# Optimization experiments

Measured on AMD Instinct MI355X. Metric: run time of the kernel, lower is better.

Reference implementation:

```python
import jax, jax.numpy as jnp
import numpy as np
import math

Z, H, G, S = 4, 16, 4, 4096          # batch, q heads, kv groups, seq len
BLOCK = 32                            # compression block size
NB = S // BLOCK                       # number of compressed KV blocks (128)
DQK, DV = 128, 128                    # head dims


def setup_inputs() -> dict:
    key = jax.random.key(0)
    k1, k2, k3 = jax.random.split(key, 3)
    q = jax.random.normal(k1, (Z, H, S, DQK), jnp.float32)
    k_blocks = jax.random.normal(k2, (Z, G, NB, DQK), jnp.float32)
    v_blocks = jax.random.normal(k3, (Z, G, NB, DV), jnp.float32)
    # block j covers tokens [j*BLOCK, (j+1)*BLOCK), so it 'ends' at position (j+1)*BLOCK-1
    block_ends = (jnp.arange(1, NB + 1) * BLOCK - 1).astype(jnp.int32)
    return {"q": q, "k_blocks": k_blocks, "v_blocks": v_blocks, "block_ends": block_ends}


def reference(q, k_blocks, v_blocks, block_ends):
    """NSA compression attention fwd: block-end causal masking over compressed KV blocks.
    q: [Z,H,S,Dqk]; k_blocks/v_blocks: [Z,G,NB,D]; block_ends: [NB] int.
    Query at position m attends to compressed block j iff block_ends[j] <= m.
    Rows with no valid block output zeros (matching the kernel's l_i==0 path)."""
    Zb, Hb, Sb, Dq = q.shape
    Gb = k_blocks.shape[1]
    sm_scale = 1.0 / math.sqrt(Dq)
    # GQA: head h -> kv group h // (H // G)
    qg = (q * sm_scale).reshape(Zb, Gb, Hb // Gb, Sb, Dq)
    s = jnp.einsum('zghsd,zgnd->zghsn', qg, k_blocks)        # [Z,G,H/G,S,NB]
    pos = jnp.arange(Sb)
    mask = block_ends[None, :] <= pos[:, None]               # [S,NB]
    s_masked = jnp.where(mask, s, -jnp.inf)
    m = jnp.max(s_masked, axis=-1, keepdims=True)            # online-softmax max (M)
    m_safe = jnp.where(jnp.isfinite(m), m, 0.0)
    p = jnp.where(mask, jnp.exp(s_masked - jax.lax.stop_gradient(m_safe)), 0.0)
    l = jnp.sum(p, axis=-1, keepdims=True)                   # softmax denom (exp(L-M))
    o = jnp.einsum('zghsn,zgnv->zghsv', p, v_blocks)
    o = jnp.where(l > 0, o / jnp.where(l > 0, l, 1.0), 0.0)
    return o.reshape(Zb, Hb, Sb, -1)                         # [Z,H,S,Dv]
```

## Files before the change

kernel.cpp:

```cpp
#include <hip/hip_runtime.h>


#define Zc 4
#define Hc 16
#define Gc 4
#define Sc 4096
#define NBc 128
#define Dc 128
#define VST 136

typedef __attribute__((ext_vector_type(8))) short short8;
typedef __attribute__((ext_vector_type(4))) float float4v;

__device__ inline unsigned pk2bf(float a, float b) {
    union { float f; unsigned u; } x, y; x.f = a; y.f = b;
    return __builtin_amdgcn_perm(y.u + 0x8000u, x.u + 0x8000u, 0x07060302u);
}

__device__ inline short8 mkfrag(float4v f0, float4v f1) {
    union { short8 v; unsigned d[4]; } u;
    u.d[0] = pk2bf(f0[0], f0[1]);
    u.d[1] = pk2bf(f0[2], f0[3]);
    u.d[2] = pk2bf(f1[0], f1[1]);
    u.d[3] = pk2bf(f1[2], f1[3]);
    return u.v;
}

__global__ __launch_bounds__(256, 4)
void nsa_fwd(const float* __restrict__ q, const float* __restrict__ kb,
             const float* __restrict__ vb, float* __restrict__ out) {
    __shared__ __align__(16) short Vt[Dc * VST];

    const int m0   = blockIdx.x * 128;
    const int h    = blockIdx.y;
    const int z    = blockIdx.z;
    const int g    = h >> 2;
    const int tid  = threadIdx.x;
    const int wq   = tid >> 6;
    const int lane = tid & 63;
    const int l16  = lane & 15;
    const int quad = lane >> 4;

    const float* vsrc = vb + (size_t)(z * Gc + g) * NBc * Dc;
    #pragma unroll
    for (int it = 0; it < 16; it++) {
        int i = it * 256 + tid;
        int c = i >> 7, n = i & 127;
        float4v f = *(const float4v*)(vsrc + (size_t)n * Dc + c * 4);
        #pragma unroll
        for (int k2 = 0; k2 < 4; k2++) {
            union { float f; unsigned u; } x; x.f = f[k2];
            Vt[(c * 4 + k2) * VST + n] = (short)((x.u + 0x8000u) >> 16);
        }
    }

    const float* ksrc  = kb + (size_t)(z * Gc + g) * NBc * Dc;
    const float* qbase = q + ((size_t)(z * Hc + h) * Sc + m0 + wq * 32) * Dc;

    float4v acc[8][2];
    #pragma unroll
    for (int c = 0; c < 8; c++)
        #pragma unroll
        for (int t = 0; t < 2; t++) acc[c][t] = (float4v)0.f;

    #pragma unroll
    for (int dk = 0; dk < 4; dk++) {
        const int d0 = dk * 32 + quad * 8;
        short8 bq[2];
        #pragma unroll
        for (int t = 0; t < 2; t++) {
            const float* s = qbase + (size_t)(t * 16 + l16) * Dc + d0;
            bq[t] = mkfrag(*(const float4v*)s, *(const float4v*)(s + 4));
        }
        #pragma unroll
        for (int c = 0; c < 8; c++) {
            const float* s = ksrc + (size_t)(c * 16 + l16) * Dc + d0;
            short8 a = mkfrag(*(const float4v*)s, *(const float4v*)(s + 4));
            #pragma unroll
            for (int t = 0; t < 2; t++)
                acc[c][t] = __builtin_amdgcn_mfma_f32_16x16x32_bf16(
                    a, bq[t], acc[c][t], 0, 0, 0);
        }
    }

    const float sm_scale = 0.08838834764831845f;
    unsigned Ppk[8][2][2];
    #pragma unroll
    for (int t = 0; t < 2; t++) {
        const int mg = m0 + wq * 32 + t * 16 + l16;
        int nv = (mg + 1) >> 5; if (nv > NBc) nv = NBc;
        float mx = -1e30f;
        #pragma unroll
        for (int c = 0; c < 8; c++)
            #pragma unroll
            for (int r = 0; r < 4; r++) {
                const int j = c * 16 + quad * 4 + r;
                float s = acc[c][t][r] * sm_scale;
                s = (j < nv) ? s : -1e30f;
                acc[c][t][r] = s;
                mx = fmaxf(mx, s);
            }
        mx = fmaxf(mx, __shfl_xor(mx, 16, 64));
        mx = fmaxf(mx, __shfl_xor(mx, 32, 64));
        float ls = 0.f;
        #pragma unroll
        for (int c = 0; c < 8; c++)
            #pragma unroll
            for (int r = 0; r < 4; r++) {
                float s = acc[c][t][r];
                float p = (s > -1e29f) ? __expf(s - mx) : 0.f;
                acc[c][t][r] = p;
                ls += p;
            }
        ls += __shfl_xor(ls, 16, 64);
        ls += __shfl_xor(ls, 32, 64);
        const float inv = (ls > 0.f) ? 1.f / ls : 0.f;
        #pragma unroll
        for (int c = 0; c < 8; c++) {
            Ppk[c][t][0] = pk2bf(acc[c][t][0] * inv, acc[c][t][1] * inv);
            Ppk[c][t][1] = pk2bf(acc[c][t][2] * inv, acc[c][t][3] * inv);
        }
    }

    __syncthreads();

    float4v oacc[8][2];
    #pragma unroll
    for (int c = 0; c < 8; c++)
        #pragma unroll
        for (int t = 0; t < 2; t++) oacc[c][t] = (float4v)0.f;

    const int s0 = (((2 * quad) & 3) << 4) | l16;
    const int s1 = (((2 * quad + 1) & 3) << 4) | l16;
    const bool hi = (quad >= 2);

    #pragma unroll
    for (int kbi = 0; kbi < 4; kbi++) {
        short8 ap[2];
        #pragma unroll
        for (int t = 0; t < 2; t++) {
            const int c1 = 2 * kbi;
            unsigned w0a = (unsigned)__shfl((int)Ppk[c1    ][t][0], s0, 64);
            unsigned w0b = (unsigned)__shfl((int)Ppk[c1 + 1][t][0], s0, 64);
            unsigned w1a = (unsigned)__shfl((int)Ppk[c1    ][t][1], s0, 64);
            unsigned w1b = (unsigned)__shfl((int)Ppk[c1 + 1][t][1], s0, 64);
            unsigned w2a = (unsigned)__shfl((int)Ppk[c1    ][t][0], s1, 64);
            unsigned w2b = (unsigned)__shfl((int)Ppk[c1 + 1][t][0], s1, 64);
            unsigned w3a = (unsigned)__shfl((int)Ppk[c1    ][t][1], s1, 64);
            unsigned w3b = (unsigned)__shfl((int)Ppk[c1 + 1][t][1], s1, 64);
            union { short8 v; unsigned d[4]; } u;
            u.d[0] = hi ? w0b : w0a;
            u.d[1] = hi ? w1b : w1a;
            u.d[2] = hi ? w2b : w2a;
            u.d[3] = hi ? w3b : w3a;
            ap[t] = u.v;
        }
        #pragma unroll
        for (int c = 0; c < 8; c++) {
            short8 bv = *(const short8*)(Vt + (c * 16 + l16) * VST + kbi * 32 + quad * 8);
            #pragma unroll
            for (int t = 0; t < 2; t++)
                oacc[c][t] = __builtin_amdgcn_mfma_f32_16x16x32_bf16(
                    ap[t], bv, oacc[c][t], 0, 0, 0);
        }
    }

    float* obase = out + ((size_t)(z * Hc + h) * Sc + m0 + wq * 32) * Dc;
    #pragma unroll
    for (int t = 0; t < 2; t++)
        #pragma unroll
        for (int rr = 0; rr < 4; rr++) {
            const int row = t * 16 + quad * 4 + rr;
            #pragma unroll
            for (int c = 0; c < 8; c++)
                obase[(size_t)row * Dc + c * 16 + l16] = oacc[c][t][rr];
        }
}

extern "C" void kernel_launch(void* const* d_in, const int* in_sizes, int n_in,
                              void* d_out, int out_size, void* d_ws, size_t ws_size,
                              hipStream_t stream) {
    const float* q  = (const float*)d_in[0];
    const float* kb = (const float*)d_in[1];
    const float* vb = (const float*)d_in[2];
    float* out = (float*)d_out;
    dim3 grid(Sc / 128, Hc, Zc);
    nsa_fwd<<<grid, dim3(256), 0, stream>>>(q, kb, vb, out);
}
```

Before: 296.1 us.

## Stage bf16 K in shared memory, preload Q, and skip causally masked blocks

K blocks are converted to bf16 once per workgroup into shared memory instead of each wave reloading and converting them from global memory. Q fragments are loaded early and pre-scaled by the softmax scale. Per-tile bounds derived from the causal block mask skip QK and PV MFMAs and softmax work for key blocks that are fully masked. The cost is doubled LDS use and occupancy lowered from 4 to 2 blocks per CU in launch bounds, plus more registers held for the preloaded Q.

```diff
diff --git a/kernel.cpp b/kernel.cpp
--- a/kernel.cpp
+++ b/kernel.cpp
@@ -16,7 +16,6 @@
     union { float f; unsigned u; } x, y; x.f = a; y.f = b;
     return __builtin_amdgcn_perm(y.u + 0x8000u, x.u + 0x8000u, 0x07060302u);
 }
-
 __device__ inline short8 mkfrag(float4v f0, float4v f1) {
     union { short8 v; unsigned d[4]; } u;
     u.d[0] = pk2bf(f0[0], f0[1]);
@@ -26,21 +25,44 @@
     return u.v;
 }
 
-__global__ __launch_bounds__(256, 4)
+__global__ __launch_bounds__(256, 2)
 void nsa_fwd(const float* __restrict__ q, const float* __restrict__ kb,
              const float* __restrict__ vb, float* __restrict__ out) {
+    __shared__ __align__(16) short Ksh[NBc * VST];
     __shared__ __align__(16) short Vt[Dc * VST];
 
-    const int m0   = blockIdx.x * 128;
-    const int h    = blockIdx.y;
-    const int z    = blockIdx.z;
-    const int g    = h >> 2;
+    const int bx   = blockIdx.x, m0 = bx * 128;
+    const int h    = blockIdx.y, z = blockIdx.z, g = h >> 2;
     const int tid  = threadIdx.x;
     const int wq   = tid >> 6;
     const int lane = tid & 63;
     const int l16  = lane & 15;
     const int quad = lane >> 4;
 
+    const int nvmax   = 4 * bx + 4;
+    const int c_max   = (nvmax + 15) >> 4;
+    const int kbi_max = (nvmax + 31) >> 5;
+
+    const float* qbase = q + ((size_t)(z * Hc + h) * Sc + m0 + wq * 32) * Dc;
+    float4v qraw[4][2][2];
+    #pragma unroll
+    for (int dk = 0; dk < 4; dk++)
+        #pragma unroll
+        for (int t = 0; t < 2; t++) {
+            const float* s = qbase + (size_t)(t * 16 + l16) * Dc + dk * 32 + quad * 8;
+            qraw[dk][t][0] = *(const float4v*)s;
+            qraw[dk][t][1] = *(const float4v*)(s + 4);
+        }
+
+    const float* ksrc = kb + (size_t)(z * Gc + g) * NBc * Dc;
+    #pragma unroll
+    for (int it = 0; it < 8; it++) {
+        int i = it * 256 + tid;
+        int n = i >> 4, c8 = i & 15;
+        const float* s = ksrc + (size_t)n * Dc + c8 * 8;
+        float4v f0 = *(const float4v*)s, f1 = *(const float4v*)(s + 4);
+        *(short8*)(Ksh + n * VST + c8 * 8) = mkfrag(f0, f1);
+    }
     const float* vsrc = vb + (size_t)(z * Gc + g) * NBc * Dc;
     #pragma unroll
     for (int it = 0; it < 16; it++) {
@@ -54,8 +76,15 @@
         }
     }
 
-    const float* ksrc  = kb + (size_t)(z * Gc + g) * NBc * Dc;
-    const float* qbase = q + ((size_t)(z * Hc + h) * Sc + m0 + wq * 32) * Dc;
+    const float sm = 0.08838834764831845f;
+    short8 qf[4][2];
+    #pragma unroll
+    for (int dk = 0; dk < 4; dk++)
+        #pragma unroll
+        for (int t = 0; t < 2; t++)
+            qf[dk][t] = mkfrag(qraw[dk][t][0] * sm, qraw[dk][t][1] * sm);
+
+    __syncthreads();
 
     float4v acc[8][2];
     #pragma unroll
@@ -64,27 +93,21 @@
         for (int t = 0; t < 2; t++) acc[c][t] = (float4v)0.f;
 
     #pragma unroll
-    for (int dk = 0; dk < 4; dk++) {
-        const int d0 = dk * 32 + quad * 8;
-        short8 bq[2];
-        #pragma unroll
-        for (int t = 0; t < 2; t++) {
-            const float* s = qbase + (size_t)(t * 16 + l16) * Dc + d0;
-            bq[t] = mkfrag(*(const float4v*)s, *(const float4v*)(s + 4));
-        }
-        #pragma unroll
-        for (int c = 0; c < 8; c++) {
-            const float* s = ksrc + (size_t)(c * 16 + l16) * Dc + d0;
-            short8 a = mkfrag(*(const float4v*)s, *(const float4v*)(s + 4));
-            #pragma unroll
-            for (int t = 0; t < 2; t++)
-                acc[c][t] = __builtin_amdgcn_mfma_f32_16x16x32_bf16(
-                    a, bq[t], acc[c][t], 0, 0, 0);
-        }
-    }
-
-    const float sm_scale = 0.08838834764831845f;
+    for (int dk = 0; dk < 4; dk++)
+        #pragma unroll
+        for (int c = 0; c < 8; c++)
+            if (c < c_max) {
+                short8 a = *(const short8*)(Ksh + (c * 16 + l16) * VST + dk * 32 + quad * 8);
+                acc[c][0] = __builtin_amdgcn_mfma_f32_16x16x32_bf16(a, qf[dk][0], acc[c][0], 0, 0, 0);
+                acc[c][1] = __builtin_amdgcn_mfma_f32_16x16x32_bf16(a, qf[dk][1], acc[c][1], 0, 0, 0);
+            }
+
     unsigned Ppk[8][2][2];
+    #pragma unroll
+    for (int c = 0; c < 8; c++)
+        #pragma unroll
+        for (int t = 0; t < 2; t++) { Ppk[c][t][0] = 0u; Ppk[c][t][1] = 0u; }
+
     #pragma unroll
     for (int t = 0; t < 2; t++) {
         const int mg = m0 + wq * 32 + t * 16 + l16;
@@ -92,37 +115,38 @@
         float mx = -1e30f;
         #pragma unroll
         for (int c = 0; c < 8; c++)
-            #pragma unroll
-            for (int r = 0; r < 4; r++) {
-                const int j = c * 16 + quad * 4 + r;
-                float s = acc[c][t][r] * sm_scale;
-                s = (j < nv) ? s : -1e30f;
-                acc[c][t][r] = s;
-                mx = fmaxf(mx, s);
-            }
+            if (c < c_max)
+                #pragma unroll
+                for (int r = 0; r < 4; r++) {
+                    const int j = c * 16 + quad * 4 + r;
+                    float s = acc[c][t][r];
+                    s = (j < nv) ? s : -1e30f;
+                    acc[c][t][r] = s;
+                    mx = fmaxf(mx, s);
+                }
         mx = fmaxf(mx, __shfl_xor(mx, 16, 64));
         mx = fmaxf(mx, __shfl_xor(mx, 32, 64));
         float ls = 0.f;
         #pragma unroll
         for (int c = 0; c < 8; c++)
-            #pragma unroll
-            for (int r = 0; r < 4; r++) {
-                float s = acc[c][t][r];
-                float p = (s > -1e29f) ? __expf(s - mx) : 0.f;
-                acc[c][t][r] = p;
-                ls += p;
-            }
+            if (c < c_max)
+                #pragma unroll
+                for (int r = 0; r < 4; r++) {
+                    float s = acc[c][t][r];
+                    float p = (s > -1e29f) ? __expf(s - mx) : 0.f;
+                    acc[c][t][r] = p;
+                    ls += p;
+                }
         ls += __shfl_xor(ls, 16, 64);
         ls += __shfl_xor(ls, 32, 64);
         const float inv = (ls > 0.f) ? 1.f / ls : 0.f;
         #pragma unroll
-        for (int c = 0; c < 8; c++) {
-            Ppk[c][t][0] = pk2bf(acc[c][t][0] * inv, acc[c][t][1] * inv);
-            Ppk[c][t][1] = pk2bf(acc[c][t][2] * inv, acc[c][t][3] * inv);
-        }
+        for (int c = 0; c < 8; c++)
+            if (c < c_max) {
+                Ppk[c][t][0] = pk2bf(acc[c][t][0] * inv, acc[c][t][1] * inv);
+                Ppk[c][t][1] = pk2bf(acc[c][t][2] * inv, acc[c][t][3] * inv);
+            }
     }
-
-    __syncthreads();
 
     float4v oacc[8][2];
     #pragma unroll
@@ -135,35 +159,35 @@
     const bool hi = (quad >= 2);
 
     #pragma unroll
-    for (int kbi = 0; kbi < 4; kbi++) {
-        short8 ap[2];
-        #pragma unroll
-        for (int t = 0; t < 2; t++) {
-            const int c1 = 2 * kbi;
-            unsigned w0a = (unsigned)__shfl((int)Ppk[c1    ][t][0], s0, 64);
-            unsigned w0b = (unsigned)__shfl((int)Ppk[c1 + 1][t][0], s0, 64);
-            unsigned w1a = (unsigned)__shfl((int)Ppk[c1    ][t][1], s0, 64);
-            unsigned w1b = (unsigned)__shfl((int)Ppk[c1 + 1][t][1], s0, 64);
-            unsigned w2a = (unsigned)__shfl((int)Ppk[c1    ][t][0], s1, 64);
-            unsigned w2b = (unsigned)__shfl((int)Ppk[c1 + 1][t][0], s1, 64);
-            unsigned w3a = (unsigned)__shfl((int)Ppk[c1    ][t][1], s1, 64);
-            unsigned w3b = (unsigned)__shfl((int)Ppk[c1 + 1][t][1], s1, 64);
-            union { short8 v; unsigned d[4]; } u;
-            u.d[0] = hi ? w0b : w0a;
-            u.d[1] = hi ? w1b : w1a;
-            u.d[2] = hi ? w2b : w2a;
-            u.d[3] = hi ? w3b : w3a;
-            ap[t] = u.v;
-        }
-        #pragma unroll
-        for (int c = 0; c < 8; c++) {
-            short8 bv = *(const short8*)(Vt + (c * 16 + l16) * VST + kbi * 32 + quad * 8);
+    for (int kbi = 0; kbi < 4; kbi++)
+        if (kbi < kbi_max) {
+            short8 ap[2];
             #pragma unroll
-            for (int t = 0; t < 2; t++)
-                oacc[c][t] = __builtin_amdgcn_mfma_f32_16x16x32_bf16(
-                    ap[t], bv, oacc[c][t], 0, 0, 0);
-        }
-    }
+            for (int t = 0; t < 2; t++) {
+                const int c1 = 2 * kbi;
+                unsigned w0a = (unsigned)__shfl((int)Ppk[c1    ][t][0], s0, 64);
+                unsigned w0b = (unsigned)__shfl((int)Ppk[c1 + 1][t][0], s0, 64);
+                unsigned w1a = (unsigned)__shfl((int)Ppk[c1    ][t][1], s0, 64);
+                unsigned w1b = (unsigned)__shfl((int)Ppk[c1 + 1][t][1], s0, 64);
+                unsigned w2a = (unsigned)__shfl((int)Ppk[c1    ][t][0], s1, 64);
+                unsigned w2b = (unsigned)__shfl((int)Ppk[c1 + 1][t][0], s1, 64);
+                unsigned w3a = (unsigned)__shfl((int)Ppk[c1    ][t][1], s1, 64);
+                unsigned w3b = (unsigned)__shfl((int)Ppk[c1 + 1][t][1], s1, 64);
+                union { short8 v; unsigned d[4]; } u;
+                u.d[0] = hi ? w0b : w0a;
+                u.d[1] = hi ? w1b : w1a;
+                u.d[2] = hi ? w2b : w2a;
+                u.d[3] = hi ? w3b : w3a;
+                ap[t] = u.v;
+            }
+            #pragma unroll
+            for (int c = 0; c < 8; c++) {
+                short8 bv = *(const short8*)(Vt + (c * 16 + l16) * VST + kbi * 32 + quad * 8);
+                #pragma unroll
+                for (int t = 0; t < 2; t++)
+                    oacc[c][t] = __builtin_amdgcn_mfma_f32_16x16x32_bf16(ap[t], bv, oacc[c][t], 0, 0, 0);
+            }
+        }
 
     float* obase = out + ((size_t)(z * Hc + h) * Sc + m0 + wq * 32) * Dc;
     #pragma unroll
```

Measured after the change: 252.7 us. 14.6% less time.
